# Kernel optimization log

Measured on AMD Instinct MI355X. Metric: run time of the kernel, lower is better.

Reference implementation:

```python
import jax, jax.numpy as jnp
import numpy as np

N_QUBITS = 11
N_LAYERS = 5
N3 = 3 * N_QUBITS
DIM = 1 << N_QUBITS
C64 = jnp.complex64

CNOT4 = jnp.array([[1., 0., 0., 0.],
                   [0., 1., 0., 0.],
                   [0., 0., 0., 1.],
                   [0., 0., 1., 0.]], dtype=C64)

def _ry(t):
    c, s = jnp.cos(0.5 * t), jnp.sin(0.5 * t)
    return jnp.stack([jnp.stack([c, -s]), jnp.stack([s, c])]).astype(C64)

def _rz(t):
    e = jnp.exp(-0.5j * t.astype(C64))
    z = jnp.zeros((), C64)
    return jnp.stack([jnp.stack([e, z]), jnp.stack([z, jnp.conj(e)])])

def apply_1q(psi, U, q):
    # psi: [B, 2, ..., 2]; qubit 0 is the most-significant axis (kron order lst[0] x lst[1] x ...)
    psi = jnp.moveaxis(psi, 1 + q, -1)
    if U.ndim == 2:
        psi = psi @ U.T
    else:  # per-batch gate [B, 2, 2]
        psi = jnp.einsum('b...j,bij->b...i', psi, U)
    return jnp.moveaxis(psi, -1, 1 + q)

def apply_cnot(psi, c, t):
    psi = jnp.moveaxis(psi, (1 + c, 1 + t), (-2, -1))
    sh = psi.shape
    psi = (psi.reshape(sh[:-2] + (4,)) @ CNOT4.T).reshape(sh)
    return jnp.moveaxis(psi, (-2, -1), (1 + c, 1 + t))

def yzy_layer(psi, params):
    # per-qubit param triples: Ry(p0) Rz(p1) Ry(p2)
    p = params.reshape(N_QUBITS, 3)
    for q in range(N_QUBITS):
        psi = apply_1q(psi, _ry(p[q, 0]), q)
        psi = apply_1q(psi, _rz(p[q, 1]), q)
        psi = apply_1q(psi, _ry(p[q, 2]), q)
    return psi

def _forward(x, w, dimA):
    B = x.shape[0]
    # |0...0> initial state as a [B, 2]*n tensor
    psi = jnp.zeros((B,) + (2,) * N_QUBITS, C64).at[(slice(None),) + (0,) * N_QUBITS].set(1.0)
    # angle embedding, axis='Y': m = cos(x/2) I - i sin(x/2) Y = real rotation matrix
    half = 0.5 * x[:, 0, :]                     # [B, n]
    c, s = jnp.cos(half), jnp.sin(half)
    for q in range(N_QUBITS):
        U = jnp.stack([jnp.stack([c[:, q], -s[:, q]], -1),
                       jnp.stack([s[:, q], c[:, q]], -1)], -2).astype(C64)  # [B,2,2]
        psi = apply_1q(psi, U, q)
    # variational circuit: (YZYLayer + ring_of_cnot) * n_layers + final YZYLayer
    for layer in range(N_LAYERS):
        psi = yzy_layer(psi, w[layer * N3:(layer + 1) * N3])
        for q in range(N_QUBITS):
            psi = apply_cnot(psi, q, (q + 1) % N_QUBITS)
    psi = yzy_layer(psi, w[N_LAYERS * N3:])
    state = psi.reshape(B, DIM)
    # DM = psi psi^dagger, then partial trace over first dimB (most-significant) qubits
    dm = jnp.einsum('bi,bj->bij', state, jnp.conj(state))   # [B, DIM, DIM]
    dB = 1 << (N_QUBITS - dimA)
    dA = 1 << dimA
    return jnp.einsum('bijik->bjk', dm.reshape(B, dB, dA, dB, dA))

def setup_inputs():
    key = jax.random.key(0)
    k1, k2 = jax.random.split(key)
    x = jax.random.uniform(k1, (16, 1, N_QUBITS), jnp.float32, 0.0, 2 * np.pi)
    w_scale = (2 ** 0.5) * 5 ** (-0.5)  # he_std * w_mul with use_wscale=True, lrmul=1
    w = jax.random.uniform(k2, (N3 * (N_LAYERS + 1),), jnp.float32, 0.0, 2 * np.pi) * w_scale
    return {"x": x, "w": w, "dimA": 5}

def reference(x, w, dimA):
    return _forward(x, w, dimA)
```

## Files before the change

kernel.cpp:

```cpp
#include <hip/hip_runtime.h>

#define NQ 11
#define DIM 2048
#define NL 5
#define NLAYERS 6
#define NGATES (NLAYERS * NQ)

struct c32 { float re, im; };

__device__ __forceinline__ c32 cmul(c32 a, c32 b) {
    return { a.re * b.re - a.im * b.im, a.re * b.im + a.im * b.re };
}
__device__ __forceinline__ c32 cmadd(c32 acc, c32 a, c32 b) {
    return { fmaf(a.re, b.re, fmaf(-a.im, b.im, acc.re)),
             fmaf(a.re, b.im, fmaf(a.im, b.re, acc.im)) };
}

__device__ __forceinline__ int ring_perm(int u) {
    int P = u ^ (u >> 1);
    P ^= P >> 2;
    P ^= P >> 4;
    P ^= P >> 8;
    return (P & 0x3FF) | (((P ^ (u >> 10)) & 1) << 10);
}

__global__ __launch_bounds__(1024) void qsim_kernel(
    const float* __restrict__ x,
    const float* __restrict__ w,
    float* __restrict__ out)
{
    __shared__ c32 psi[DIM];
    __shared__ c32 gates[NGATES][4];

    const int b = blockIdx.x;
    const int t = threadIdx.x;

    if (t < NGATES) {
        const int l = t / NQ, q = t % NQ;
        const float* p = &w[l * 3 * NQ + q * 3];
        float c0, s0, cz, sz, c2, s2;
        sincosf(0.5f * p[0], &s0, &c0);
        sincosf(0.5f * p[1], &sz, &cz);
        sincosf(0.5f * p[2], &s2, &c2);
        c32 A00 = {  cz * c0, -sz * c0 };
        c32 A01 = { -cz * s0,  sz * s0 };
        c32 A10 = {  cz * s0,  sz * s0 };
        c32 A11 = {  cz * c0,  sz * c0 };
        c32 M00 = { c2 * A00.re - s2 * A10.re, c2 * A00.im - s2 * A10.im };
        c32 M01 = { c2 * A01.re - s2 * A11.re, c2 * A01.im - s2 * A11.im };
        c32 M10 = { s2 * A00.re + c2 * A10.re, s2 * A00.im + c2 * A10.im };
        c32 M11 = { s2 * A01.re + c2 * A11.re, s2 * A01.im + c2 * A11.im };
        if (l == 0) {
            float ce, se;
            sincosf(0.5f * x[b * NQ + q], &se, &ce);
            c32 N00 = { M00.re * ce + M01.re * se, M00.im * ce + M01.im * se };
            c32 N01 = { M01.re * ce - M00.re * se, M01.im * ce - M00.im * se };
            c32 N10 = { M10.re * ce + M11.re * se, M10.im * ce + M11.im * se };
            c32 N11 = { M11.re * ce - M10.re * se, M11.im * ce - M10.im * se };
            M00 = N00; M01 = N01; M10 = N10; M11 = N11;
        }
        gates[t][0] = M00; gates[t][1] = M01;
        gates[t][2] = M10; gates[t][3] = M11;
    }

    psi[t]        = { (t == 0) ? 1.f : 0.f, 0.f };
    psi[t + 1024] = { 0.f, 0.f };
    __syncthreads();

    for (int l = 0; l < NLAYERS; l++) {
        for (int q = 0; q < NQ; q++) {
            const int bp = 10 - q;
            const int lo = t & ((1 << bp) - 1);
            const int i0 = ((t >> bp) << (bp + 1)) | lo;
            const int i1 = i0 | (1 << bp);
            const c32 m00 = gates[l * NQ + q][0];
            const c32 m01 = gates[l * NQ + q][1];
            const c32 m10 = gates[l * NQ + q][2];
            const c32 m11 = gates[l * NQ + q][3];
            const c32 a0 = psi[i0];
            const c32 a1 = psi[i1];
            psi[i0] = cmadd(cmul(m00, a0), m01, a1);
            psi[i1] = cmadd(cmul(m10, a0), m11, a1);
            __syncthreads();
        }
        if (l < NL) {
            const c32 v0 = psi[t];
            const c32 v1 = psi[t + 1024];
            const int d0 = ring_perm(t);
            const int d1 = ring_perm(t + 1024);
            __syncthreads();
            psi[d0] = v0;
            psi[d1] = v1;
            __syncthreads();
        }
    }

    const int j = t >> 5, k = t & 31;
    float re = 0.f, im = 0.f;
#pragma unroll 8
    for (int i = 0; i < 64; i++) {
        const c32 a = psi[i * 32 + j];
        const c32 c = psi[i * 32 + k];
        re = fmaf(a.re, c.re, fmaf(a.im, c.im, re));
        im = fmaf(a.im, c.re, fmaf(-a.re, c.im, im));
    }
    out[b * 1024 + t]         = re;
    out[16384 + b * 1024 + t] = im;
}

extern "C" void kernel_launch(void* const* d_in, const int* in_sizes, int n_in,
                              void* d_out, int out_size, void* d_ws, size_t ws_size,
                              hipStream_t stream) {
    const float* x = (const float*)d_in[0];
    const float* w = (const float*)d_in[1];
    float* out = (float*)d_out;
    qsim_kernel<<<16, 1024, 0, stream>>>(x, w, out);
}
```

Before: 80.16 us.

## Keep state in registers and fold CNOT ring into GF(2) basis changes

Each of 256 threads now holds 8 amplitudes in registers. The CNOT-ring permutations are absorbed algebraically: each gate acts on a compile-time GF(2) mask and row computed with constexpr, and is applied through in-register pairing, wave shuffles, or a shared-memory exchange only when the mask crosses waves. This removes the per-gate __syncthreads and shared-memory round trips, plus the explicit permutation passes. The final partial trace uses 2x2 register tiling per thread. The cost is heavy template unrolling that may raise register pressure and code size, with 256 threads instead of 1024.

```diff
diff --git a/kernel.cpp b/kernel.cpp
--- a/kernel.cpp
+++ b/kernel.cpp
@@ -2,41 +2,150 @@
 
 #define NQ 11
 #define DIM 2048
-#define NL 5
-#define NLAYERS 6
-#define NGATES (NLAYERS * NQ)
+#define NLAY 6
+#define NGATES (NLAY * NQ)
 
 struct c32 { float re, im; };
 
-__device__ __forceinline__ c32 cmul(c32 a, c32 b) {
-    return { a.re * b.re - a.im * b.im, a.re * b.im + a.im * b.re };
-}
-__device__ __forceinline__ c32 cmadd(c32 acc, c32 a, c32 b) {
-    return { fmaf(a.re, b.re, fmaf(-a.im, b.im, acc.re)),
-             fmaf(a.re, b.im, fmaf(a.im, b.re, acc.im)) };
-}
-
-__device__ __forceinline__ int ring_perm(int u) {
-    int P = u ^ (u >> 1);
-    P ^= P >> 2;
-    P ^= P >> 4;
-    P ^= P >> 8;
+__host__ __device__ constexpr int ring_f(int u) {
+    int P = u ^ (u >> 1); P ^= P >> 2; P ^= P >> 4; P ^= P >> 8;
     return (P & 0x3FF) | (((P ^ (u >> 10)) & 1) << 10);
 }
-
-__global__ __launch_bounds__(1024) void qsim_kernel(
+__host__ __device__ constexpr int ring_inv(int v) {
+    int o = 0;
+    for (int i = 0; i < 9; i++) o |= (((v >> i) ^ (v >> (i + 1))) & 1) << i;
+    o |= (((v >> 0) ^ (v >> 9) ^ (v >> 10)) & 1) << 9;
+    o |= (((v >> 0) ^ (v >> 10)) & 1) << 10;
+    return o;
+}
+__host__ __device__ constexpr int ring_pow(int v, int k)     { for (int i = 0; i < k; i++) v = ring_f(v);   return v; }
+__host__ __device__ constexpr int ring_inv_pow(int v, int k) { for (int i = 0; i < k; i++) v = ring_inv(v); return v; }
+__host__ __device__ constexpr int par11(int x) { x ^= x >> 8; x ^= x >> 4; x ^= x >> 2; x ^= x >> 1; return x & 1; }
+
+__host__ __device__ constexpr int mask_of(int L, int b) { return ring_inv_pow(1 << b, L); }
+__host__ __device__ constexpr int row_of(int L, int b) {
+    int m = 0;
+    for (int j = 0; j < 11; j++) m |= ((ring_pow(1 << j, L) >> b) & 1) << j;
+    return m;
+}
+__host__ __device__ constexpr int cgate_index(int L, int Q) {
+    int n = 0;
+    for (int l = 0; l <= L; l++)
+        for (int q = 0; q < (l < L ? NQ : Q); q++)
+            if (mask_of(l, 10 - q) >> 9) n++;
+    return n;
+}
+constexpr bool gf2_checks() {
+    for (int u = 0; u < DIM; u++)
+        if (ring_inv(ring_f(u)) != u || ring_f(ring_inv(u)) != u) return false;
+    for (int l = 0; l < NLAY; l++)
+        for (int q = 0; q < NQ; q++) {
+            const int b = 10 - q;
+            if (mask_of(l, b) == 0) return false;
+            if (par11(mask_of(l, b) & row_of(l, b)) != 1) return false;
+        }
+    return true;
+}
+static_assert(gf2_checks(), "GF2 ring algebra broken");
+
+struct RP5T { int v[8]; };
+__host__ __device__ constexpr RP5T mkRP5() { RP5T t{}; for (int r = 0; r < 8; r++) t.v[r] = ring_pow(r, 5); return t; }
+constexpr RP5T RP5 = mkRP5();
+
+__device__ __forceinline__ c32 comb(c32 cA, c32 xx, c32 cB, c32 yy) {
+    float re =  cA.re * xx.re;
+    re = fmaf(-cA.im, xx.im, re);
+    re = fmaf( cB.re, yy.re, re);
+    re = fmaf(-cB.im, yy.im, re);
+    float im =  cA.re * xx.im;
+    im = fmaf( cA.im, xx.re, im);
+    im = fmaf( cB.re, yy.im, im);
+    im = fmaf( cB.im, yy.re, im);
+    return { re, im };
+}
+
+template<int L, int Q>
+__device__ __forceinline__ void do_gate(c32 (&a)[8], const c32 (&g)[4],
+                                        c32* exA, c32* exB, int tid) {
+    constexpr int b     = 10 - Q;
+    constexpr int M     = mask_of(L, b);
+    constexpr int RW    = row_of(L, b);
+    constexpr int mr    = M & 7;
+    constexpr int mt    = M >> 3;
+    constexpr int mlane = mt & 63;
+    constexpr int mwav  = mt >> 6;
+
+    const c32 m00 = g[0], m01 = g[1], m10 = g[2], m11 = g[3];
+    const int sl = __popc(tid & (RW >> 3)) & 1;
+    const c32 cO0 = sl ? m11 : m00, cP0 = sl ? m10 : m01;
+    const c32 cO1 = sl ? m00 : m11, cP1 = sl ? m01 : m10;
+
+    if constexpr (mwav != 0) {
+        c32* buf = (cgate_index(L, Q) & 1) ? exB : exA;
+#pragma unroll
+        for (int r = 0; r < 8; r++) buf[(r << 8) | tid] = a[r];
+        __syncthreads();
+#pragma unroll
+        for (int r = 0; r < 8; r++) {
+            const c32 pv = buf[((r ^ mr) << 8) | (tid ^ mt)];
+            const int cr = __popc(r & (RW & 7)) & 1;
+            a[r] = cr ? comb(cO1, a[r], cP1, pv) : comb(cO0, a[r], cP0, pv);
+        }
+    } else if constexpr (mlane != 0 && mr == 0) {
+#pragma unroll
+        for (int r = 0; r < 8; r++) {
+            const c32 pv { __shfl_xor(a[r].re, mlane, 64), __shfl_xor(a[r].im, mlane, 64) };
+            const int cr = __popc(r & (RW & 7)) & 1;
+            a[r] = cr ? comb(cO1, a[r], cP1, pv) : comb(cO0, a[r], cP0, pv);
+        }
+    } else if constexpr (mlane != 0) {
+        constexpr int piv = mr & (-mr);
+#pragma unroll
+        for (int r0 = 0; r0 < 8; r0++) if (!(r0 & piv)) {
+            const int r1 = r0 ^ mr;
+            const c32 o0 = a[r0], o1 = a[r1];
+            const c32 pv0 { __shfl_xor(o1.re, mlane, 64), __shfl_xor(o1.im, mlane, 64) };
+            const c32 pv1 { __shfl_xor(o0.re, mlane, 64), __shfl_xor(o0.im, mlane, 64) };
+            const int cr0 = __popc(r0 & (RW & 7)) & 1;
+            const int cr1 = cr0 ^ (__popc(mr & (RW & 7)) & 1);
+            a[r0] = cr0 ? comb(cO1, o0, cP1, pv0) : comb(cO0, o0, cP0, pv0);
+            a[r1] = cr1 ? comb(cO1, o1, cP1, pv1) : comb(cO0, o1, cP0, pv1);
+        }
+    } else {
+        constexpr int piv = mr & (-mr);
+#pragma unroll
+        for (int r0 = 0; r0 < 8; r0++) if (!(r0 & piv)) {
+            const int r1 = r0 ^ mr;
+            const c32 o0 = a[r0], o1 = a[r1];
+            const int cr0 = __popc(r0 & (RW & 7)) & 1;
+            a[r0] = cr0 ? comb(cO1, o0, cP1, o1) : comb(cO0, o0, cP0, o1);
+            a[r1] = cr0 ? comb(cO0, o1, cP0, o0) : comb(cO1, o1, cP1, o0);
+        }
+    }
+}
+
+template<int L, int Q>
+__device__ __forceinline__ void run_gates(c32 (&a)[8], const c32 (*gates)[4],
+                                          c32* exA, c32* exB, int tid) {
+    do_gate<L, Q>(a, gates[L * NQ + Q], exA, exB, tid);
+    if constexpr (Q < NQ - 1)       run_gates<L, Q + 1>(a, gates, exA, exB, tid);
+    else if constexpr (L < NLAY - 1) run_gates<L + 1, 0>(a, gates, exA, exB, tid);
+}
+
+__global__ __launch_bounds__(256) void qsim_kernel(
     const float* __restrict__ x,
     const float* __restrict__ w,
     float* __restrict__ out)
 {
-    __shared__ c32 psi[DIM];
+    __shared__ c32 exA[DIM];
+    __shared__ c32 exB[DIM];
     __shared__ c32 gates[NGATES][4];
 
     const int b = blockIdx.x;
-    const int t = threadIdx.x;
-
-    if (t < NGATES) {
-        const int l = t / NQ, q = t % NQ;
+    const int tid = threadIdx.x;
+
+    if (tid < NGATES) {
+        const int l = tid / NQ, q = tid % NQ;
         const float* p = &w[l * 3 * NQ + q * 3];
         float c0, s0, cz, sz, c2, s2;
         sincosf(0.5f * p[0], &s0, &c0);
@@ -59,53 +168,52 @@
             c32 N11 = { M11.re * ce - M10.re * se, M11.im * ce - M10.im * se };
             M00 = N00; M01 = N01; M10 = N10; M11 = N11;
         }
-        gates[t][0] = M00; gates[t][1] = M01;
-        gates[t][2] = M10; gates[t][3] = M11;
+        gates[tid][0] = M00; gates[tid][1] = M01;
+        gates[tid][2] = M10; gates[tid][3] = M11;
     }
 
-    psi[t]        = { (t == 0) ? 1.f : 0.f, 0.f };
-    psi[t + 1024] = { 0.f, 0.f };
+    c32 a[8];
+#pragma unroll
+    for (int r = 0; r < 8; r++) a[r] = { 0.f, 0.f };
+    if (tid == 0) a[0].re = 1.f;
     __syncthreads();
 
-    for (int l = 0; l < NLAYERS; l++) {
-        for (int q = 0; q < NQ; q++) {
-            const int bp = 10 - q;
-            const int lo = t & ((1 << bp) - 1);
-            const int i0 = ((t >> bp) << (bp + 1)) | lo;
-            const int i1 = i0 | (1 << bp);
-            const c32 m00 = gates[l * NQ + q][0];
-            const c32 m01 = gates[l * NQ + q][1];
-            const c32 m10 = gates[l * NQ + q][2];
-            const c32 m11 = gates[l * NQ + q][3];
-            const c32 a0 = psi[i0];
-            const c32 a1 = psi[i1];
-            psi[i0] = cmadd(cmul(m00, a0), m01, a1);
-            psi[i1] = cmadd(cmul(m10, a0), m11, a1);
-            __syncthreads();
-        }
-        if (l < NL) {
-            const c32 v0 = psi[t];
-            const c32 v1 = psi[t + 1024];
-            const int d0 = ring_perm(t);
-            const int d1 = ring_perm(t + 1024);
-            __syncthreads();
-            psi[d0] = v0;
-            psi[d1] = v1;
-            __syncthreads();
-        }
-    }
-
-    const int j = t >> 5, k = t & 31;
-    float re = 0.f, im = 0.f;
+    run_gates<0, 0>(a, gates, exA, exB, tid);
+
+    __syncthreads();
+    int T = tid << 3;
+#pragma unroll
+    for (int k = 0; k < 5; k++) T = ring_f(T);
+#pragma unroll
+    for (int r = 0; r < 8; r++) exA[T ^ RP5.v[r]] = a[r];
+    __syncthreads();
+
+    const int j0 = (tid >> 4) << 1, k0 = (tid & 15) << 1;
+    float r00re = 0.f, r00im = 0.f, r01re = 0.f, r01im = 0.f;
+    float r10re = 0.f, r10im = 0.f, r11re = 0.f, r11im = 0.f;
 #pragma unroll 8
     for (int i = 0; i < 64; i++) {
-        const c32 a = psi[i * 32 + j];
-        const c32 c = psi[i * 32 + k];
-        re = fmaf(a.re, c.re, fmaf(a.im, c.im, re));
-        im = fmaf(a.im, c.re, fmaf(-a.re, c.im, im));
+        const c32 A0 = exA[i * 32 + j0], A1 = exA[i * 32 + j0 + 1];
+        const c32 B0 = exA[i * 32 + k0], B1 = exA[i * 32 + k0 + 1];
+        r00re = fmaf(A0.re, B0.re, fmaf( A0.im, B0.im, r00re));
+        r00im = fmaf(A0.im, B0.re, fmaf(-A0.re, B0.im, r00im));
+        r01re = fmaf(A0.re, B1.re, fmaf( A0.im, B1.im, r01re));
+        r01im = fmaf(A0.im, B1.re, fmaf(-A0.re, B1.im, r01im));
+        r10re = fmaf(A1.re, B0.re, fmaf( A1.im, B0.im, r10re));
+        r10im = fmaf(A1.im, B0.re, fmaf(-A1.re, B0.im, r10im));
+        r11re = fmaf(A1.re, B1.re, fmaf( A1.im, B1.im, r11re));
+        r11im = fmaf(A1.im, B1.re, fmaf(-A1.re, B1.im, r11im));
     }
-    out[b * 1024 + t]         = re;
-    out[16384 + b * 1024 + t] = im;
+    float* o = out + b * 1024;
+    o[ j0      * 32 + k0    ] = r00re;
+    o[ j0      * 32 + k0 + 1] = r01re;
+    o[(j0 + 1) * 32 + k0    ] = r10re;
+    o[(j0 + 1) * 32 + k0 + 1] = r11re;
+    o += 16384;
+    o[ j0      * 32 + k0    ] = r00im;
+    o[ j0      * 32 + k0 + 1] = r01im;
+    o[(j0 + 1) * 32 + k0    ] = r10im;
+    o[(j0 + 1) * 32 + k0 + 1] = r11im;
 }
 
 extern "C" void kernel_launch(void* const* d_in, const int* in_sizes, int n_in,
@@ -114,5 +222,5 @@
     const float* x = (const float*)d_in[0];
     const float* w = (const float*)d_in[1];
     float* out = (float*)d_out;
-    qsim_kernel<<<16, 1024, 0, stream>>>(x, w, out);
-}
+    qsim_kernel<<<16, 256, 0, stream>>>(x, w, out);
+}
```

After: 77.78 us. 1.03x faster.
